# Kernel tuning notes

Hardware: AMD Instinct MI355X
Metric: run time of the kernel (lower is better)

The kernel has to match this reference:

```python
import jax, jax.numpy as jnp
import numpy as np
import math

B, N, C = 16, 4096, 256
HEADS, HD, SR, FF = 8, 32, 4, 3


def _ln(x, g, b):
    mu = jnp.mean(x, -1, keepdims=True)
    var = jnp.mean((x - mu) ** 2, -1, keepdims=True)
    return (x - mu) / jnp.sqrt(var + 1e-5) * g + b


def _interp(v, out):
    # torch F.interpolate(mode='linear', align_corners=False) along axis 1 of (B,L,C)
    L = v.shape[1]
    c = jnp.clip((jnp.arange(out, dtype=v.dtype) + 0.5) * (L / out) - 0.5, 0.0, L - 1.0)
    i0 = jnp.floor(c).astype(jnp.int32)
    i1 = jnp.minimum(i0 + 1, L - 1)
    w = (c - i0.astype(v.dtype))[None, :, None]
    return v[:, i0] * (1.0 - w) + v[:, i1] * w


def _conv(x, w, b, stride, pad=0, groups=1):
    y = jax.lax.conv_general_dilated(x, w, (stride, stride), ((pad, pad), (pad, pad)),
                                     feature_group_count=groups,
                                     dimension_numbers=('NCHW', 'OIHW', 'NCHW'))
    return y + b[None, :, None, None]


def _lin_attn(q_bhnd, k, v, pe, scale_sp, Wdwc, bdwc, n_kv):
    # NOTE: raw reshape (B,h,N,d)->(B,N,C) as in the torch source (layout quirk kept)
    q = q_bhnd.reshape(B, N, C)
    k = k + pe
    q = jax.nn.relu(q) + 1e-6
    k = jax.nn.relu(k) + 1e-6
    q = q / scale_sp
    k = k / scale_sp
    qn = jnp.linalg.norm(q, axis=-1, keepdims=True)
    kn = jnp.linalg.norm(k, axis=-1, keepdims=True)
    q = q ** FF
    k = k ** FF
    q = q / jnp.linalg.norm(q, axis=-1, keepdims=True) * qn
    k = k / jnp.linalg.norm(k, axis=-1, keepdims=True) * kn
    q = q.reshape(B, N, HEADS, HD).transpose(0, 2, 1, 3)        # (B,h,N,d)
    k = k.reshape(B, n_kv, HEADS, HD).transpose(0, 2, 1, 3)     # (B,h,n,d)
    v = v.reshape(B, n_kv, HEADS, HD).transpose(0, 2, 1, 3)
    km = jnp.mean(k, axis=2)                                     # (B,h,d)
    z = 1.0 / (jnp.einsum('bhnd,bhd->bhn', q, km) + 1e-6)
    s = N ** -0.5
    kv = jnp.einsum('bhnd,bhne->bhde', k * s, v * s)             # (B,h,d,d)
    x = jnp.einsum('bhnd,bhde->bhne', q, kv) * z[..., None]
    v2 = _interp(v.reshape(B, n_kv, C), N)                       # raw reshape quirk kept
    Hs = int(math.isqrt(N))
    x = x.transpose(0, 2, 1, 3).reshape(B, N, C)
    v2 = v2.reshape(B * HEADS, Hs, Hs, HD).transpose(0, 3, 1, 2)  # raw reshape quirk kept
    dv = _conv(v2, Wdwc, bdwc, 1, pad=2, groups=HD).reshape(B, C, N).transpose(0, 2, 1)
    return x + dv


def reference(x, Wq, bq, Wsr1, bsr1, g1, b1, Wsr2, bsr2, g2, b2,
              Wkv1, bkv1, Wkv2, bkv2, pe1, pe2, Wproj, bproj,
              Wdwc, bdwc, scale, H, W):
    q = (x @ Wq.T + bq).reshape(B, N, HEADS, HD).transpose(0, 2, 1, 3)
    x_ = x.transpose(0, 2, 1).reshape(B, C, H, W)
    x1 = jax.nn.gelu(_ln(_conv(x_, Wsr1, bsr1, SR).reshape(B, C, -1).transpose(0, 2, 1), g1, b1), approximate=False)
    x2 = jax.nn.gelu(_ln(_conv(x_, Wsr2, bsr2, SR // 2).reshape(B, C, -1).transpose(0, 2, 1), g2, b2), approximate=False)
    h1, h2 = H // SR, 2 * H // SR
    # 1x1 kv convs as linears; then replicate torch's raw reshape of the NCHW conv output
    y1 = (x1.reshape(B, h1, h1, C) @ Wkv1.T + bkv1).transpose(0, 3, 1, 2).reshape(B, h1, h1, 2 * C).reshape(B, -1, 2, C)
    y2 = (x2.reshape(B, h2, h2, C) @ Wkv2.T + bkv2).transpose(0, 3, 1, 2).reshape(B, h2, h2, 2 * C).reshape(B, -1, 2, C)
    k1, v1 = y1[:, :, 0], y1[:, :, 1]
    k2, v2 = y2[:, :, 0], y2[:, :, 1]
    scale_sp = jax.nn.softplus(scale)
    a1 = _lin_attn(q, k1, v1, pe1, scale_sp, Wdwc, bdwc, N // SR ** 2)
    a2 = _lin_attn(q, k2, v2, pe2, scale_sp, Wdwc, bdwc, 4 * N // SR ** 2)
    return jnp.concatenate([a1, a2], axis=-1) @ Wproj.T + bproj


def setup_inputs() -> dict:
    key = jax.random.key(0)
    ks = jax.random.split(key, 12)
    r = lambda k, s: jax.random.normal(k, s, dtype=jnp.float32) * 0.02
    z = lambda s: jnp.zeros(s, jnp.float32)
    return dict(
        x=jax.random.normal(ks[0], (B, N, C), dtype=jnp.float32),
        Wq=r(ks[1], (C, C)), bq=z((C,)),
        Wsr1=r(ks[2], (C, C, SR, SR)), bsr1=z((C,)),
        g1=jnp.ones((C,), jnp.float32), b1=z((C,)),
        Wsr2=r(ks[3], (C, C, SR // 2, SR // 2)), bsr2=z((C,)),
        g2=jnp.ones((C,), jnp.float32), b2=z((C,)),
        Wkv1=r(ks[4], (2 * C, C)), bkv1=z((2 * C,)),
        Wkv2=r(ks[5], (2 * C, C)), bkv2=z((2 * C,)),
        pe1=r(ks[6], (1, N // (SR * SR), C)),
        pe2=r(ks[7], (1, 4 * N // (SR * SR), C)),
        Wproj=r(ks[8], (C, 2 * C)), bproj=z((C,)),
        Wdwc=r(ks[9], (HD, 1, 5, 5)), bdwc=z((HD,)),
        scale=r(ks[10], (1, 1, C)),
        H=64, W=64,
    )
```

## Files before the change

### kernel.cpp

```cpp
#include <hip/hip_runtime.h>
#include <hip/hip_bf16.h>
#include <cmath>

constexpr int cB = 16;
constexpr int cN = 4096;
constexpr int cC = 256;

typedef __attribute__((ext_vector_type(8))) short short8;
typedef __attribute__((ext_vector_type(4))) float f32x4;

__device__ inline unsigned short bfr(float f) {
  __hip_bfloat16 h = __float2bfloat16(f);
  return *(unsigned short*)&h;
}
__device__ inline float u16tof(unsigned short u) {
  unsigned int v = ((unsigned int)u) << 16;
  return __builtin_bit_cast(float, v);
}

constexpr size_t oWQB    = 0;
constexpr size_t oW1B    = oWQB    + 32768;
constexpr size_t oW2B    = oW1B    + 524288;
constexpr size_t oWKV1B  = oW2B    + 131072;
constexpr size_t oWKV2B  = oWKV1B  + 65536;
constexpr size_t oWPROJB = oWKV2B  + 65536;
constexpr size_t oINVSP  = oWPROJB + 65536;
constexpr size_t oKM1    = oINVSP  + 1024;
constexpr size_t oKV1M   = oKM1    + 4096;
constexpr size_t oKM2    = oKV1M   + 131072;
constexpr size_t oKV2M   = oKM2    + 4096;
constexpr size_t oKVP    = oKV2M   + 131072;
constexpr size_t oKMP    = oKVP    + 524288;
constexpr size_t oQBUF   = oKMP    + 16384;
constexpr size_t oV1G    = oQBUF   + 16777216;
constexpr size_t oV2G    = oV1G    + 1048576;
constexpr size_t oU      = oV2G    + 4194304;
constexpr size_t oP1     = oU;
constexpr size_t oX1B    = oU + 4194304;
constexpr size_t oY1     = oU + 4718592;
constexpr size_t oK1P    = oU;
constexpr size_t oX2     = oU;
constexpr size_t oY2     = oU  + 4194304;
constexpr size_t oX2B    = oU  + 12582912;
constexpr size_t oK2P    = oU;
constexpr size_t oAB     = oU;

__global__ void cast_bf16_k(const float* __restrict__ src, __hip_bfloat16* __restrict__ dst, int n) {
  int idx = blockIdx.x*256 + threadIdx.x;
  if (idx < n) dst[idx] = __float2bfloat16(src[idx]);
}

__global__ void pack_conv_bf16(const float* __restrict__ src, __hip_bfloat16* __restrict__ dst, int KHW) {
  int idx = blockIdx.x*256 + threadIdx.x;
  if (idx >= 65536*KHW) return;
  int ci = idx & 255;
  int rest = idx >> 8;
  int p = rest % KHW, co = rest / KHW;
  dst[idx] = __float2bfloat16(src[((size_t)co*256 + ci)*KHW + p]);
}

__global__ void softplus_inv_k(const float* __restrict__ s, float* __restrict__ inv) {
  int c = threadIdx.x;
  float v = s[c];
  float sp = (v > 20.f) ? v : log1pf(expf(v));
  inv[c] = 1.f/sp;
}

template<int TM, int TN, int AMODE, int ADT, int EPI>
__global__ __launch_bounds__(256) void gmfma(
    const void* __restrict__ Asrc, const __hip_bfloat16* __restrict__ Bp,
    const float* __restrict__ bias, float* __restrict__ Cout,
    int M, int N, int K, int ldb)
{
  constexpr int APASS = TM/32, BPASS = TN/32;
  constexpr int WGM = (TM==128) ? 2 : ((TN==64) ? 2 : 1);
  constexpr int WGN = 4/WGM;
  constexpr int WM = TM/WGM, WN = TN/WGN;
  constexpr int FM = WM/16, FN = WN/16;
  __shared__ char smem[(TM+TN)*128];
  char* As = smem;
  char* Bs = smem + TM*128;
  const int tid  = threadIdx.x;
  const int row0 = blockIdx.x * TM;
  const int col0 = blockIdx.y * TN;
  const int kbase = blockIdx.z * K;
  const int kq = tid & 7, rl = tid >> 3;
  const int w = tid >> 6, lane = tid & 63;
  const int wr = (WGM==2) ? (w>>1) : 0;
  const int wc = (WGM==2) ? (w&1)  : w;

  f32x4 acc[FM][FN] = {};
  short8 aS[APASS], bS[BPASS];

  auto loadA = [&](int k0) {
    int ka = kbase + k0;
    #pragma unroll
    for (int p = 0; p < APASS; ++p) {
      int r = row0 + rl + p*32;
      const char* ap;
      if (AMODE == 0) {
        if (ADT == 0) ap = (const char*)((const float*)Asrc + (size_t)r*K + k0 + kq*8);
        else          ap = (const char*)((const __hip_bfloat16*)Asrc + (size_t)r*K + k0 + kq*8);
      } else if (AMODE == 1) {
        int b = r >> 8, mm = r & 255;
        int my = mm >> 4, mx = mm & 15;
        int ch = ka >> 8, ky = ch >> 2, kx = ch & 3;
        int tok = (4*my + ky)*64 + 4*mx + kx;
        ap = (const char*)((const float*)Asrc + ((size_t)(b*4096 + tok))*256 + (ka & 255) + kq*8);
      } else {
        int b = r >> 10, mm = r & 1023;
        int my = mm >> 5, mx = mm & 31;
        int ch = ka >> 8, ky = ch >> 1, kx = ch & 1;
        int tok = (2*my + ky)*64 + 2*mx + kx;
        ap = (const char*)((const float*)Asrc + ((size_t)(b*4096 + tok))*256 + (ka & 255) + kq*8);
      }
      if (ADT == 0) {
        float4 v0 = *(const float4*)ap;
        float4 v1 = *(const float4*)(ap + 16);
        short8 s;
        s[0] = (short)bfr(v0.x); s[1] = (short)bfr(v0.y);
        s[2] = (short)bfr(v0.z); s[3] = (short)bfr(v0.w);
        s[4] = (short)bfr(v1.x); s[5] = (short)bfr(v1.y);
        s[6] = (short)bfr(v1.z); s[7] = (short)bfr(v1.w);
        aS[p] = s;
      } else {
        aS[p] = *(const short8*)ap;
      }
    }
  };
  auto loadB = [&](int k0) {
    #pragma unroll
    for (int p = 0; p < BPASS; ++p) {
      int n = col0 + rl + p*32;
      bS[p] = *(const short8*)(Bp + (size_t)n*ldb + kbase + k0 + kq*8);
    }
  };

  loadA(0); loadB(0);
  for (int k0 = 0; k0 < K; k0 += 64) {
    #pragma unroll
    for (int p = 0; p < APASS; ++p) {
      int r = rl + p*32;
      *(short8*)(As + r*128 + ((kq*16) ^ ((r&7)<<4))) = aS[p];
    }
    #pragma unroll
    for (int p = 0; p < BPASS; ++p) {
      int n = rl + p*32;
      *(short8*)(Bs + n*128 + ((kq*16) ^ ((n&7)<<4))) = bS[p];
    }
    __syncthreads();
    if (k0 + 64 < K) { loadA(k0 + 64); loadB(k0 + 64); }
    #pragma unroll
    for (int ks = 0; ks < 2; ++ks) {
      short8 af[FM], bfv[FN];
      #pragma unroll
      for (int i = 0; i < FM; ++i) {
        int r = wr*WM + i*16 + (lane & 15);
        af[i] = *(const short8*)(As + r*128 + ((ks*64 + (lane>>4)*16) ^ ((r&7)<<4)));
      }
      #pragma unroll
      for (int j = 0; j < FN; ++j) {
        int n = wc*WN + j*16 + (lane & 15);
        bfv[j] = *(const short8*)(Bs + n*128 + ((ks*64 + (lane>>4)*16) ^ ((n&7)<<4)));
      }
      #pragma unroll
      for (int i = 0; i < FM; ++i)
        #pragma unroll
        for (int j = 0; j < FN; ++j)
          acc[i][j] = __builtin_amdgcn_mfma_f32_16x16x32_bf16(af[i], bfv[j], acc[i][j], 0, 0, 0);
    }
    __syncthreads();
  }

  #pragma unroll
  for (int i = 0; i < FM; ++i) {
    #pragma unroll
    for (int j = 0; j < FN; ++j) {
      int cc = col0 + wc*WN + j*16 + (lane & 15);
      float bval = (EPI == 2 || EPI == 3) ? 0.f : bias[cc];
      #pragma unroll
      for (int rg = 0; rg < 4; ++rg) {
        int rr = row0 + wr*WM + i*16 + (lane>>4)*4 + rg;
        float v = acc[i][j][rg] + bval;
        if (EPI == 0) {
          Cout[(size_t)rr*N + cc] = v;
        } else if (EPI == 1) {
          int b = rr >> 12, n = rr & 4095;
          int h = cc >> 5, d = cc & 31;
          Cout[((size_t)(b*4096 + h*512 + (n >> 3)))*256 + (n & 7)*32 + d] = v;
        } else if (EPI == 2) {
          Cout[(size_t)rr*N + cc] += v;
        } else if (EPI == 3) {
          Cout[(size_t)blockIdx.z*((size_t)M*N) + (size_t)rr*N + cc] = v;
        } else {
          int b = rr >> 12, n = rr & 4095;
          int h = cc >> 5, d = cc & 31;
          ((__hip_bfloat16*)Cout)[((size_t)(b*4096 + h*512 + (n >> 3)))*256 + (n & 7)*32 + d] =
              __float2bfloat16(v);
        }
      }
    }
  }
}

__global__ __launch_bounds__(256) void row_powernorm(float* __restrict__ x,
    const float* __restrict__ inv_sp, int rows)
{
  int row = blockIdx.x*4 + (threadIdx.x >> 6);
  if (row >= rows) return;
  int lane = threadIdx.x & 63;
  float* p = x + (size_t)row*256 + lane*4;
  float4 v = *(float4*)p;
  const float4 is = *(const float4*)(inv_sp + lane*4);
  float r0 = (fmaxf(v.x,0.f)+1e-6f)*is.x;
  float r1 = (fmaxf(v.y,0.f)+1e-6f)*is.y;
  float r2 = (fmaxf(v.z,0.f)+1e-6f)*is.z;
  float r3 = (fmaxf(v.w,0.f)+1e-6f)*is.w;
  float s2 = r0*r0+r1*r1+r2*r2+r3*r3;
  #pragma unroll
  for (int o = 1; o < 64; o <<= 1) s2 += __shfl_xor(s2, o, 64);
  float c0 = r0*r0*r0, c1 = r1*r1*r1, c2 = r2*r2*r2, c3 = r3*r3*r3;
  float s6 = c0*c0+c1*c1+c2*c2+c3*c3;
  #pragma unroll
  for (int o = 1; o < 64; o <<= 1) s6 += __shfl_xor(s6, o, 64);
  float f = sqrtf(s2/s6);
  v.x = c0*f; v.y = c1*f; v.z = c2*f; v.w = c3*f;
  *(float4*)p = v;
}

__global__ __launch_bounds__(256) void ln_gelu_sum4(const float* __restrict__ P,
    const float* __restrict__ bias, const float* __restrict__ g, const float* __restrict__ bb,
    __hip_bfloat16* __restrict__ outb, int rows)
{
  const size_t PS = (size_t)rows*256;
  int row = blockIdx.x*4 + (threadIdx.x >> 6);
  if (row >= rows) return;
  int lane = threadIdx.x & 63;
  const float* p = P + (size_t)row*256 + lane*4;
  float4 v0 = *(const float4*)p;
  float4 v1 = *(const float4*)(p + PS);
  float4 v2 = *(const float4*)(p + 2*PS);
  float4 v3 = *(const float4*)(p + 3*PS);
  float4 bsv = *(const float4*)(bias + lane*4);
  float4 v;
  v.x = v0.x+v1.x+v2.x+v3.x+bsv.x;
  v.y = v0.y+v1.y+v2.y+v3.y+bsv.y;
  v.z = v0.z+v1.z+v2.z+v3.z+bsv.z;
  v.w = v0.w+v1.w+v2.w+v3.w+bsv.w;
  float s = v.x+v.y+v.z+v.w;
  #pragma unroll
  for (int o = 1; o < 64; o <<= 1) s += __shfl_xor(s, o, 64);
  float mu = s*(1.f/256.f);
  float d0 = v.x-mu, d1 = v.y-mu, d2 = v.z-mu, d3 = v.w-mu;
  float q = d0*d0+d1*d1+d2*d2+d3*d3;
  #pragma unroll
  for (int o = 1; o < 64; o <<= 1) q += __shfl_xor(q, o, 64);
  float rstd = rsqrtf(q*(1.f/256.f) + 1e-5f);
  float4 gv = *(const float4*)(g + lane*4);
  float4 bv = *(const float4*)(bb + lane*4);
  float y0 = d0*rstd*gv.x + bv.x;
  float y1 = d1*rstd*gv.y + bv.y;
  float y2 = d2*rstd*gv.z + bv.z;
  float y3 = d3*rstd*gv.w + bv.w;
  const float k = 0.70710678118654752f;
  ushort4 u;
  u.x = bfr(0.5f*y0*(1.f+erff(y0*k)));
  u.y = bfr(0.5f*y1*(1.f+erff(y1*k)));
  u.z = bfr(0.5f*y2*(1.f+erff(y2*k)));
  u.w = bfr(0.5f*y3*(1.f+erff(y3*k)));
  *(ushort4*)(outb + (size_t)row*256 + lane*4) = u;
}

__global__ __launch_bounds__(256) void ln_gelu_b(const float* __restrict__ x,
    const float* __restrict__ g, const float* __restrict__ bb,
    __hip_bfloat16* __restrict__ outb, int rows)
{
  int row = blockIdx.x*4 + (threadIdx.x >> 6);
  if (row >= rows) return;
  int lane = threadIdx.x & 63;
  const float* p = x + (size_t)row*256 + lane*4;
  float4 v = *(const float4*)p;
  float s = v.x+v.y+v.z+v.w;
  #pragma unroll
  for (int o = 1; o < 64; o <<= 1) s += __shfl_xor(s, o, 64);
  float mu = s*(1.f/256.f);
  float d0 = v.x-mu, d1 = v.y-mu, d2 = v.z-mu, d3 = v.w-mu;
  float q = d0*d0+d1*d1+d2*d2+d3*d3;
  #pragma unroll
  for (int o = 1; o < 64; o <<= 1) q += __shfl_xor(q, o, 64);
  float rstd = rsqrtf(q*(1.f/256.f) + 1e-5f);
  float4 gv = *(const float4*)(g + lane*4);
  float4 bv = *(const float4*)(bb + lane*4);
  float y0 = d0*rstd*gv.x + bv.x;
  float y1 = d1*rstd*gv.y + bv.y;
  float y2 = d2*rstd*gv.z + bv.z;
  float y3 = d3*rstd*gv.w + bv.w;
  const float k = 0.70710678118654752f;
  ushort4 u;
  u.x = bfr(0.5f*y0*(1.f+erff(y0*k)));
  u.y = bfr(0.5f*y1*(1.f+erff(y1*k)));
  u.z = bfr(0.5f*y2*(1.f+erff(y2*k)));
  u.w = bfr(0.5f*y3*(1.f+erff(y3*k)));
  *(ushort4*)(outb + (size_t)row*256 + lane*4) = u;
}

template<int BR>
__global__ __launch_bounds__(256) void gather_kv2(const float* __restrict__ y,
    const float* __restrict__ pe, float* __restrict__ Ko, float* __restrict__ Vo)
{
  constexpr int NKV = (BR == 1) ? 256 : 1024;
  __shared__ float tk[64][65];
  __shared__ float tv[64][65];
  int bid = blockIdx.x;
  int cb = bid & 3;
  int nb = (bid >> 2) % (NKV/64);
  int b  = (bid >> 2) / (NKV/64);
  int n0 = nb*64, c0 = cb*64;
  int tid = threadIdx.x;
  #pragma unroll
  for (int pass = 0; pass < 16; ++pass) {
    int c_l = (tid >> 6)*16 + pass;
    int c = c0 + c_l;
    if (BR == 1) {
      int n_l = tid & 63;
      size_t base = ((size_t)(b*256 + c))*512 + 2*(n0 + n_l);
      tk[c_l][n_l] = y[base];
      tv[c_l][n_l] = y[base + 1];
    } else {
      int u = tid & 31, pp = (tid >> 5) & 1;
      int n_l = 2*u + pp;
      size_t rk = ((size_t)(b*1024 + pp*512 + c))*512 + (size_t)((n0 >> 1) + u);
      tk[c_l][n_l] = y[rk];
      tv[c_l][n_l] = y[rk + (size_t)256*512];
    }
  }
  __syncthreads();
  #pragma unroll
  for (int pass = 0; pass < 16; ++pass) {
    int n_l = (tid >> 6)*16 + pass;
    int c_l = tid & 63;
    int n = n0 + n_l, c = c0 + c_l;
    size_t o = ((size_t)(b*NKV + n))*256 + c;
    Ko[o] = tk[c_l][n_l] + pe[n*256 + c];
    Vo[o] = tv[c_l][n_l];
  }
}

__global__ __launch_bounds__(256) void kmkv_part(const float* __restrict__ kp,
    const float* __restrict__ vg, float* __restrict__ kmp, float* __restrict__ kvp, int nkv)
{
  int g = blockIdx.x;
  int ch = g & 3, bh = g >> 2;
  int b = bh >> 3, h = bh & 7;
  int nchunk = nkv >> 2;
  int tid = threadIdx.x;
  __shared__ float ks[64][32];
  __shared__ float vs[64][32];
  int d  = tid >> 3;
  int e0 = (tid & 7)*4;
  float acc[4] = {0.f,0.f,0.f,0.f};
  float kmacc = 0.f;
  for (int n0 = ch*nchunk; n0 < (ch+1)*nchunk; n0 += 64) {
    #pragma unroll
    for (int i = 0; i < 2; ++i) {
      int f = tid + i*256;
      int nn = f >> 3, q4 = (f & 7)*4;
      size_t base = ((size_t)(b*nkv + n0 + nn))*256 + h*32 + q4;
      *(float4*)&ks[nn][q4] = *(const float4*)(kp + base);
      *(float4*)&vs[nn][q4] = *(const float4*)(vg + base);
    }
    __syncthreads();
    #pragma unroll 8
    for (int nn = 0; nn < 64; ++nn) {
      float kd = ks[nn][d];
      kmacc += kd;
      #pragma unroll
      for (int j = 0; j < 4; ++j) acc[j] += kd * vs[nn][e0+j];
    }
    __syncthreads();
  }
  const float s2c = 1.0f/4096.0f;
  #pragma unroll
  for (int j = 0; j < 4; ++j)
    kvp[(size_t)ch*131072 + ((size_t)bh*32 + e0 + j)*32 + d] = acc[j]*s2c;
  if ((tid & 7) == 0) kmp[ch*4096 + bh*32 + d] = kmacc;
}

__global__ __launch_bounds__(256) void kmkv_red(const float* __restrict__ kmp,
    const float* __restrict__ kvp, float* __restrict__ km, float* __restrict__ kvm, float inv_nkv)
{
  int idx = blockIdx.x*256 + threadIdx.x;
  kvm[idx] = kvp[idx] + kvp[131072 + idx] + kvp[262144 + idx] + kvp[393216 + idx];
  if (idx < 4096)
    km[idx] = (kmp[idx] + kmp[4096 + idx] + kmp[8192 + idx] + kmp[12288 + idx]) * inv_nkv;
}

__global__ __launch_bounds__(512) void attn_mfma(const __hip_bfloat16* __restrict__ q,
    const float* __restrict__ inv_sp,
    const float* __restrict__ km1, const float* __restrict__ kv1,
    const float* __restrict__ km2, const float* __restrict__ kv2,
    __hip_bfloat16* __restrict__ A)
{
  __shared__ __align__(16) char qs[64*512];
  __shared__ __align__(16) char kvs[32*512];
  __shared__ float zsf[2*64*8];
  const int bid = blockIdx.x;
  const int b = bid >> 6, t0 = (bid & 63)*64;
  const int tid = threadIdx.x;

  {
    const float* src = kv1 + (size_t)b*8192;
    for (int i = tid; i < 8192; i += 512) {
      int h = i >> 10, e = (i >> 5) & 31, d = i & 31;
      *(unsigned short*)(kvs + e*512 + ((h*64 + d*2) ^ ((e&7)<<4))) = bfr(src[i]);
    }
  }

  {
    const int h = tid & 7;
    const int t_l = tid >> 3;
    const float* km1p = km1 + b*256 + h*32;
    const float* km2p = km2 + b*256 + h*32;
    const __hip_bfloat16* qp = q + ((size_t)(b*4096 + t0 + t_l))*256 + h*32;
    float cf[32];
    float s2 = 0.f, s6 = 0.f;
    #pragma unroll
    for (int j = 0; j < 4; ++j) {
      short8 qv = *(const short8*)(qp + j*8);
      float4 is0 = *(const float4*)(inv_sp + h*32 + j*8);
      float4 is1 = *(const float4*)(inv_sp + h*32 + j*8 + 4);
      float isv[8] = {is0.x, is0.y, is0.z, is0.w, is1.x, is1.y, is1.z, is1.w};
      #pragma unroll
      for (int k = 0; k < 8; ++k) {
        float val = u16tof((unsigned short)qv[k]);
        float r = (fmaxf(val, 0.f) + 1e-6f) * isv[k];
        s2 += r*r;
        float c = r*r*r;
        s6 += c*c;
        cf[j*8 + k] = c;
      }
    }
    #pragma unroll
    for (int o = 1; o < 8; o <<= 1) {
      s2 += __shfl_xor(s2, o, 64);
      s6 += __shfl_xor(s6, o, 64);
    }
    float f = sqrtf(s2/s6);
    float d1 = 0.f, d2 = 0.f;
    #pragma unroll
    for (int j = 0; j < 8; ++j) {
      float4 k1 = *(const float4*)(km1p + j*4);
      float4 k2 = *(const float4*)(km2p + j*4);
      float q0 = cf[4*j+0]*f, q1 = cf[4*j+1]*f, q2 = cf[4*j+2]*f, q3 = cf[4*j+3]*f;
      cf[4*j+0] = q0; cf[4*j+1] = q1; cf[4*j+2] = q2; cf[4*j+3] = q3;
      d1 += q0*k1.x + q1*k1.y + q2*k1.z + q3*k1.w;
      d2 += q0*k2.x + q1*k2.y + q2*k2.z + q3*k2.w;
    }
    zsf[0*512 + t_l*8 + h] = 1.0f/(d1 + 1e-6f);
    zsf[1*512 + t_l*8 + h] = 1.0f/(d2 + 1e-6f);
    #pragma unroll
    for (int j = 0; j < 4; ++j) {
      short8 s;
      #pragma unroll
      for (int k = 0; k < 8; ++k) s[k] = (short)bfr(cf[j*8+k]);
      *(short8*)(qs + t_l*512 + ((h*64 + j*16) ^ ((t_l&7)<<4))) = s;
    }
  }
  __syncthreads();

  const int h = tid >> 6, l = tid & 63;
  const int lr = l & 15, lk = l >> 4;
  #pragma unroll
  for (int br = 0; br < 2; ++br) {
    if (br == 1) {
      __syncthreads();
      const float* src = kv2 + (size_t)b*8192;
      for (int i = tid; i < 8192; i += 512) {
        int hh = i >> 10, e = (i >> 5) & 31, d = i & 31;
        *(unsigned short*)(kvs + e*512 + ((hh*64 + d*2) ^ ((e&7)<<4))) = bfr(src[i]);
      }
      __syncthreads();
    }
    #pragma unroll
    for (int tt = 0; tt < 4; ++tt) {
      int tr = tt*16 + lr;
      short8 af = *(const short8*)(qs + tr*512 + ((h*64 + lk*16) ^ ((tr&7)<<4)));
      #pragma unroll
      for (int eb = 0; eb < 2; ++eb) {
        int e = eb*16 + lr;
        short8 bf = *(const short8*)(kvs + e*512 + ((h*64 + lk*16) ^ ((e&7)<<4)));
        f32x4 acc = {0.f, 0.f, 0.f, 0.f};
        acc = __builtin_amdgcn_mfma_f32_16x16x32_bf16(af, bf, acc, 0, 0, 0);
        #pragma unroll
        for (int rg = 0; rg < 4; ++rg) {
          int row = lk*4 + rg;
          float z = zsf[br*512 + (tt*16 + row)*8 + h];
          A[((size_t)(b*4096 + t0 + tt*16 + row))*512 + br*256 + h*32 + e] =
              __float2bfloat16(acc[rg]*z);
        }
      }
    }
  }
}

template<int BR>
__global__ __launch_bounds__(256) void interp_img(const float* __restrict__ vg, float* __restrict__ img) {
  constexpr int L    = (BR == 1) ? 256 : 1024;
  constexpr int RPSH = (BR == 1) ? 5 : 7;
  int row = blockIdx.x*4 + (threadIdx.x >> 6);
  int lane = threadIdx.x & 63;
  int b = row >> 12, t = row & 4095;
  float cpos = ((float)t + 0.5f) * ((float)L / 4096.0f) - 0.5f;
  cpos = fminf(fmaxf(cpos, 0.0f), (float)(L-1));
  int i0 = (int)cpos;
  float w = cpos - (float)i0;
  int i1 = (i0 + 1 < L) ? i0 + 1 : L - 1;
  int cc = lane*4;
  int n0 = ((i0 & ((L/8)-1)) << 3) + (cc >> 5), ch0 = ((i0 >> RPSH) << 5) + (cc & 31);
  int n1 = ((i1 & ((L/8)-1)) << 3) + (cc >> 5), ch1 = ((i1 >> RPSH) << 5) + (cc & 31);
  float4 v0 = *(const float4*)(vg + ((size_t)(b*L + n0))*256 + ch0);
  float4 v1 = *(const float4*)(vg + ((size_t)(b*L + n1))*256 + ch1);
  float4 o;
  o.x = v0.x + (v1.x - v0.x)*w;
  o.y = v0.y + (v1.y - v0.y)*w;
  o.z = v0.z + (v1.z - v0.z)*w;
  o.w = v0.w + (v1.w - v0.w)*w;
  size_t off = ((size_t)((b*8 + (t >> 9))*4096 + ((t >> 3) & 63)*64 + (t & 7)*8 + (cc >> 5)))*32 + (cc & 31);
  *(float4*)(img + off) = o;
}

__global__ __launch_bounds__(256) void dwconv_v3(const float* __restrict__ img,
    const float* __restrict__ Wd, const float* __restrict__ bias,
    __hip_bfloat16* __restrict__ A, int broff)
{
  int wg = blockIdx.x;
  int wid = (wg & 7)*1024 + (wg >> 3);
  int y  = wid & 63;
  int be = wid >> 6;
  int tid = threadIdx.x;
  int d = tid & 31, xg = tid >> 5;
  const float* base = img + (size_t)be*131072 + d;
  float w[25];
  #pragma unroll
  for (int i = 0; i < 25; ++i) w[i] = Wd[d*25 + i];
  float acc[8] = {};
  #pragma unroll
  for (int dy = 0; dy < 5; ++dy) {
    int yy = y + dy - 2;
    if (yy >= 0 && yy <= 63) {
      const float* rb = base + yy*2048;
      float in[12];
      #pragma unroll
      for (int i = 0; i < 12; ++i) {
        int xx = xg*8 - 2 + i;
        in[i] = (xx < 0 || xx > 63) ? 0.f : rb[xx*32];
      }
      #pragma unroll
      for (int dx = 0; dx < 5; ++dx) {
        float ww = w[dy*5 + dx];
        #pragma unroll
        for (int j = 0; j < 8; ++j) acc[j] += ww * in[j + dx];
      }
    }
  }
  int b = be >> 3, e = be & 7;
  float bv = bias[d];
  #pragma unroll
  for (int j = 0; j < 8; ++j) {
    size_t o = ((size_t)(b*4096 + y*64 + xg*8 + j))*512 + broff + e*32 + d;
    float cur = __bfloat162float(A[o]);
    A[o] = __float2bfloat16(cur + acc[j] + bv);
  }
}

extern "C" void kernel_launch(void* const* d_in, const int* in_sizes, int n_in,
                              void* d_out, int out_size, void* d_ws, size_t ws_size,
                              hipStream_t stream)
{
  (void)in_sizes; (void)n_in; (void)out_size; (void)ws_size;
  const float* x     = (const float*)d_in[0];
  const float* Wq    = (const float*)d_in[1];
  const float* bq    = (const float*)d_in[2];
  const float* Wsr1  = (const float*)d_in[3];
  const float* bsr1  = (const float*)d_in[4];
  const float* g1    = (const float*)d_in[5];
  const float* b1    = (const float*)d_in[6];
  const float* Wsr2  = (const float*)d_in[7];
  const float* bsr2  = (const float*)d_in[8];
  const float* g2    = (const float*)d_in[9];
  const float* b2    = (const float*)d_in[10];
  const float* Wkv1  = (const float*)d_in[11];
  const float* bkv1  = (const float*)d_in[12];
  const float* Wkv2  = (const float*)d_in[13];
  const float* bkv2  = (const float*)d_in[14];
  const float* pe1   = (const float*)d_in[15];
  const float* pe2   = (const float*)d_in[16];
  const float* Wproj = (const float*)d_in[17];
  const float* bproj = (const float*)d_in[18];
  const float* Wdwc  = (const float*)d_in[19];
  const float* bdwc  = (const float*)d_in[20];
  const float* scale = (const float*)d_in[21];
  float* out = (float*)d_out;
  float* ws  = (float*)d_ws;
  dim3 blk(256);

  __hip_bfloat16* WQB    = (__hip_bfloat16*)(ws + oWQB);
  __hip_bfloat16* W1B    = (__hip_bfloat16*)(ws + oW1B);
  __hip_bfloat16* W2B    = (__hip_bfloat16*)(ws + oW2B);
  __hip_bfloat16* WKV1B  = (__hip_bfloat16*)(ws + oWKV1B);
  __hip_bfloat16* WKV2B  = (__hip_bfloat16*)(ws + oWKV2B);
  __hip_bfloat16* WPROJB = (__hip_bfloat16*)(ws + oWPROJB);
  __hip_bfloat16* X1B    = (__hip_bfloat16*)(ws + oX1B);
  __hip_bfloat16* X2B    = (__hip_bfloat16*)(ws + oX2B);
  __hip_bfloat16* AB     = (__hip_bfloat16*)(ws + oAB);
  __hip_bfloat16* QB     = (__hip_bfloat16*)(ws + oQBUF);
  float*          IMGF   = (float*)(ws + oQBUF);

  cast_bf16_k<<<256,  blk, 0, stream>>>(Wq,    WQB,    65536);
  cast_bf16_k<<<512,  blk, 0, stream>>>(Wkv1,  WKV1B,  131072);
  cast_bf16_k<<<512,  blk, 0, stream>>>(Wkv2,  WKV2B,  131072);
  cast_bf16_k<<<512,  blk, 0, stream>>>(Wproj, WPROJB, 131072);
  pack_conv_bf16<<<4096, blk, 0, stream>>>(Wsr1, W1B, 16);
  pack_conv_bf16<<<1024, blk, 0, stream>>>(Wsr2, W2B, 4);
  softplus_inv_k<<<1, blk, 0, stream>>>(scale, ws + oINVSP);

  gmfma<128,128,0,0,4><<<dim3(512,2), blk, 0, stream>>>(x, WQB, bq, (float*)QB, 65536, 256, 256, 256);

  gmfma<64,64,1,0,3><<<dim3(64,4,4), blk, 0, stream>>>(x, W1B, bsr1, ws+oP1, 4096, 256, 1024, 4096);
  ln_gelu_sum4<<<1024, blk, 0, stream>>>(ws+oP1, bsr1, g1, b1, X1B, 4096);
  gmfma<64,64,0,1,0><<<dim3(64,8), blk, 0, stream>>>(X1B, WKV1B, bkv1, ws+oY1, 4096, 512, 256, 256);
  gather_kv2<1><<<256, blk, 0, stream>>>(ws+oY1, pe1, ws+oK1P, ws+oV1G);
  row_powernorm<<<1024, blk, 0, stream>>>(ws+oK1P, ws+oINVSP, 4096);
  kmkv_part<<<512, blk, 0, stream>>>(ws+oK1P, ws+oV1G, ws+oKMP, ws+oKVP, 256);
  kmkv_red<<<512, blk, 0, stream>>>(ws+oKMP, ws+oKVP, ws+oKM1, ws+oKV1M, 1.0f/256.0f);

  gmfma<64,64,2,0,0><<<dim3(256,4), blk, 0, stream>>>(x, W2B, bsr2, ws+oX2, 16384, 256, 1024, 1024);
  ln_gelu_b<<<4096, blk, 0, stream>>>(ws+oX2, g2, b2, X2B, 16384);
  gmfma<64,64,0,1,0><<<dim3(256,8), blk, 0, stream>>>(X2B, WKV2B, bkv2, ws+oY2, 16384, 512, 256, 256);
  gather_kv2<2><<<1024, blk, 0, stream>>>(ws+oY2, pe2, ws+oK2P, ws+oV2G);
  row_powernorm<<<4096, blk, 0, stream>>>(ws+oK2P, ws+oINVSP, 16384);
  kmkv_part<<<512, blk, 0, stream>>>(ws+oK2P, ws+oV2G, ws+oKMP, ws+oKVP, 1024);
  kmkv_red<<<512, blk, 0, stream>>>(ws+oKMP, ws+oKVP, ws+oKM2, ws+oKV2M, 1.0f/1024.0f);

  attn_mfma<<<1024, dim3(512), 0, stream>>>(QB, ws+oINVSP,
      ws+oKM1, ws+oKV1M, ws+oKM2, ws+oKV2M, AB);

  interp_img<1><<<16384, blk, 0, stream>>>(ws+oV1G, IMGF);
  dwconv_v3<<<cB*8*64, blk, 0, stream>>>(IMGF, Wdwc, bdwc, AB, 0);
  interp_img<2><<<16384, blk, 0, stream>>>(ws+oV2G, IMGF);
  dwconv_v3<<<cB*8*64, blk, 0, stream>>>(IMGF, Wdwc, bdwc, AB, 256);

  gmfma<128,128,0,1,0><<<dim3(512,2), blk, 0, stream>>>(AB, WPROJB, bproj, out, 65536, 256, 512, 512);
}
```

Baseline: 369.4 us.

## Merge weight packing kernels, fold km/kv reduction into attention, halve attention tile

```diff
diff --git a/kernel.cpp b/kernel.cpp
--- a/kernel.cpp
+++ b/kernel.cpp
@@ -25,13 +25,11 @@
 constexpr size_t oWKV2B  = oWKV1B  + 65536;
 constexpr size_t oWPROJB = oWKV2B  + 65536;
 constexpr size_t oINVSP  = oWPROJB + 65536;
-constexpr size_t oKM1    = oINVSP  + 1024;
-constexpr size_t oKV1M   = oKM1    + 4096;
-constexpr size_t oKM2    = oKV1M   + 131072;
-constexpr size_t oKV2M   = oKM2    + 4096;
-constexpr size_t oKVP    = oKV2M   + 131072;
-constexpr size_t oKMP    = oKVP    + 524288;
-constexpr size_t oQBUF   = oKMP    + 16384;
+constexpr size_t oKMP1   = oINVSP  + 1024;
+constexpr size_t oKVP1   = oKMP1   + 16384;
+constexpr size_t oKMP2   = oKVP1   + 524288;
+constexpr size_t oKVP2   = oKMP2   + 16384;
+constexpr size_t oQBUF   = oKVP2   + 524288;
 constexpr size_t oV1G    = oQBUF   + 16777216;
 constexpr size_t oV2G    = oV1G    + 1048576;
 constexpr size_t oU      = oV2G    + 4194304;
@@ -45,25 +43,39 @@
 constexpr size_t oK2P    = oU;
 constexpr size_t oAB     = oU;
 
-__global__ void cast_bf16_k(const float* __restrict__ src, __hip_bfloat16* __restrict__ dst, int n) {
-  int idx = blockIdx.x*256 + threadIdx.x;
-  if (idx < n) dst[idx] = __float2bfloat16(src[idx]);
-}
-
-__global__ void pack_conv_bf16(const float* __restrict__ src, __hip_bfloat16* __restrict__ dst, int KHW) {
-  int idx = blockIdx.x*256 + threadIdx.x;
-  if (idx >= 65536*KHW) return;
-  int ci = idx & 255;
-  int rest = idx >> 8;
-  int p = rest % KHW, co = rest / KHW;
-  dst[idx] = __float2bfloat16(src[((size_t)co*256 + ci)*KHW + p]);
-}
-
-__global__ void softplus_inv_k(const float* __restrict__ s, float* __restrict__ inv) {
-  int c = threadIdx.x;
-  float v = s[c];
-  float sp = (v > 20.f) ? v : log1pf(expf(v));
-  inv[c] = 1.f/sp;
+__global__ __launch_bounds__(256) void pack_all(
+    const float* __restrict__ Wq,   const float* __restrict__ Wkv1,
+    const float* __restrict__ Wkv2, const float* __restrict__ Wproj,
+    const float* __restrict__ Wsr1, const float* __restrict__ Wsr2,
+    const float* __restrict__ scale,
+    __hip_bfloat16* WQB, __hip_bfloat16* WKV1B, __hip_bfloat16* WKV2B,
+    __hip_bfloat16* WPROJB, __hip_bfloat16* W1B, __hip_bfloat16* W2B,
+    float* inv_sp)
+{
+  int bid = blockIdx.x, tid = threadIdx.x;
+  if (bid < 256) {
+    int i = bid*256 + tid; WQB[i] = __float2bfloat16(Wq[i]);
+  } else if (bid < 768) {
+    int i = (bid-256)*256 + tid; WKV1B[i] = __float2bfloat16(Wkv1[i]);
+  } else if (bid < 1280) {
+    int i = (bid-768)*256 + tid; WKV2B[i] = __float2bfloat16(Wkv2[i]);
+  } else if (bid < 1792) {
+    int i = (bid-1280)*256 + tid; WPROJB[i] = __float2bfloat16(Wproj[i]);
+  } else if (bid < 5888) {
+    int i = (bid-1792)*256 + tid;
+    int ci = i & 255, rest = i >> 8;
+    int p = rest & 15, co = rest >> 4;
+    W1B[i] = __float2bfloat16(Wsr1[((size_t)co*256 + ci)*16 + p]);
+  } else if (bid < 6912) {
+    int i = (bid-5888)*256 + tid;
+    int ci = i & 255, rest = i >> 8;
+    int p = rest & 3, co = rest >> 2;
+    W2B[i] = __float2bfloat16(Wsr2[((size_t)co*256 + ci)*4 + p]);
+  } else {
+    float v = scale[tid];
+    float sp = (v > 20.f) ? v : log1pf(expf(v));
+    inv_sp[tid] = 1.f/sp;
+  }
 }
 
 template<int TM, int TN, int AMODE, int ADT, int EPI>
@@ -386,41 +398,31 @@
   if ((tid & 7) == 0) kmp[ch*4096 + bh*32 + d] = kmacc;
 }
 
-__global__ __launch_bounds__(256) void kmkv_red(const float* __restrict__ kmp,
-    const float* __restrict__ kvp, float* __restrict__ km, float* __restrict__ kvm, float inv_nkv)
-{
-  int idx = blockIdx.x*256 + threadIdx.x;
-  kvm[idx] = kvp[idx] + kvp[131072 + idx] + kvp[262144 + idx] + kvp[393216 + idx];
-  if (idx < 4096)
-    km[idx] = (kmp[idx] + kmp[4096 + idx] + kmp[8192 + idx] + kmp[12288 + idx]) * inv_nkv;
-}
-
 __global__ __launch_bounds__(512) void attn_mfma(const __hip_bfloat16* __restrict__ q,
     const float* __restrict__ inv_sp,
-    const float* __restrict__ km1, const float* __restrict__ kv1,
-    const float* __restrict__ km2, const float* __restrict__ kv2,
+    const float* __restrict__ kmp1, const float* __restrict__ kvp1,
+    const float* __restrict__ kmp2, const float* __restrict__ kvp2,
     __hip_bfloat16* __restrict__ A)
 {
-  __shared__ __align__(16) char qs[64*512];
+  __shared__ __align__(16) char qs[32*512];
   __shared__ __align__(16) char kvs[32*512];
-  __shared__ float zsf[2*64*8];
+  __shared__ float zsf[2*32*8];
   const int bid = blockIdx.x;
-  const int b = bid >> 6, t0 = (bid & 63)*64;
+  const int b = bid >> 7, t0 = (bid & 127)*32;
   const int tid = threadIdx.x;
 
-  {
-    const float* src = kv1 + (size_t)b*8192;
-    for (int i = tid; i < 8192; i += 512) {
-      int h = i >> 10, e = (i >> 5) & 31, d = i & 31;
-      *(unsigned short*)(kvs + e*512 + ((h*64 + d*2) ^ ((e&7)<<4))) = bfr(src[i]);
-    }
-  }
-
-  {
+  for (int i = tid; i < 8192; i += 512) {
+    const float* sp = kvp1 + (size_t)b*8192 + i;
+    float v = sp[0] + sp[131072] + sp[262144] + sp[393216];
+    int h = i >> 10, e = (i >> 5) & 31, d = i & 31;
+    *(unsigned short*)(kvs + e*512 + ((h*64 + d*2) ^ ((e&7)<<4))) = bfr(v);
+  }
+
+  if (tid < 256) {
     const int h = tid & 7;
     const int t_l = tid >> 3;
-    const float* km1p = km1 + b*256 + h*32;
-    const float* km2p = km2 + b*256 + h*32;
+    const float* km1p = kmp1 + b*256 + h*32;
+    const float* km2p = kmp2 + b*256 + h*32;
     const __hip_bfloat16* qp = q + ((size_t)(b*4096 + t0 + t_l))*256 + h*32;
     float cf[32];
     float s2 = 0.f, s6 = 0.f;
@@ -449,15 +451,29 @@
     float d1 = 0.f, d2 = 0.f;
     #pragma unroll
     for (int j = 0; j < 8; ++j) {
-      float4 k1 = *(const float4*)(km1p + j*4);
-      float4 k2 = *(const float4*)(km2p + j*4);
+      float4 k1a = *(const float4*)(km1p + j*4);
+      float4 k1b = *(const float4*)(km1p + 4096 + j*4);
+      float4 k1c = *(const float4*)(km1p + 8192 + j*4);
+      float4 k1d = *(const float4*)(km1p + 12288 + j*4);
+      float4 k2a = *(const float4*)(km2p + j*4);
+      float4 k2b = *(const float4*)(km2p + 4096 + j*4);
+      float4 k2c = *(const float4*)(km2p + 8192 + j*4);
+      float4 k2d = *(const float4*)(km2p + 12288 + j*4);
+      float k1x = (k1a.x+k1b.x+k1c.x+k1d.x)*(1.f/256.f);
+      float k1y = (k1a.y+k1b.y+k1c.y+k1d.y)*(1.f/256.f);
+      float k1z = (k1a.z+k1b.z+k1c.z+k1d.z)*(1.f/256.f);
+      float k1w = (k1a.w+k1b.w+k1c.w+k1d.w)*(1.f/256.f);
+      float k2x = (k2a.x+k2b.x+k2c.x+k2d.x)*(1.f/1024.f);
+      float k2y = (k2a.y+k2b.y+k2c.y+k2d.y)*(1.f/1024.f);
+      float k2z = (k2a.z+k2b.z+k2c.z+k2d.z)*(1.f/1024.f);
+      float k2w = (k2a.w+k2b.w+k2c.w+k2d.w)*(1.f/1024.f);
       float q0 = cf[4*j+0]*f, q1 = cf[4*j+1]*f, q2 = cf[4*j+2]*f, q3 = cf[4*j+3]*f;
       cf[4*j+0] = q0; cf[4*j+1] = q1; cf[4*j+2] = q2; cf[4*j+3] = q3;
-      d1 += q0*k1.x + q1*k1.y + q2*k1.z + q3*k1.w;
-      d2 += q0*k2.x + q1*k2.y + q2*k2.z + q3*k2.w;
-    }
-    zsf[0*512 + t_l*8 + h] = 1.0f/(d1 + 1e-6f);
-    zsf[1*512 + t_l*8 + h] = 1.0f/(d2 + 1e-6f);
+      d1 += q0*k1x + q1*k1y + q2*k1z + q3*k1w;
+      d2 += q0*k2x + q1*k2y + q2*k2z + q3*k2w;
+    }
+    zsf[0*256 + t_l*8 + h] = 1.0f/(d1 + 1e-6f);
+    zsf[1*256 + t_l*8 + h] = 1.0f/(d2 + 1e-6f);
     #pragma unroll
     for (int j = 0; j < 4; ++j) {
       short8 s;
@@ -474,15 +490,16 @@
   for (int br = 0; br < 2; ++br) {
     if (br == 1) {
       __syncthreads();
-      const float* src = kv2 + (size_t)b*8192;
       for (int i = tid; i < 8192; i += 512) {
+        const float* sp = kvp2 + (size_t)b*8192 + i;
+        float v = sp[0] + sp[131072] + sp[262144] + sp[393216];
         int hh = i >> 10, e = (i >> 5) & 31, d = i & 31;
-        *(unsigned short*)(kvs + e*512 + ((hh*64 + d*2) ^ ((e&7)<<4))) = bfr(src[i]);
+        *(unsigned short*)(kvs + e*512 + ((hh*64 + d*2) ^ ((e&7)<<4))) = bfr(v);
       }
       __syncthreads();
     }
     #pragma unroll
-    for (int tt = 0; tt < 4; ++tt) {
+    for (int tt = 0; tt < 2; ++tt) {
       int tr = tt*16 + lr;
       short8 af = *(const short8*)(qs + tr*512 + ((h*64 + lk*16) ^ ((tr&7)<<4)));
       #pragma unroll
@@ -494,7 +511,7 @@
         #pragma unroll
         for (int rg = 0; rg < 4; ++rg) {
           int row = lk*4 + rg;
-          float z = zsf[br*512 + (tt*16 + row)*8 + h];
+          float z = zsf[br*256 + (tt*16 + row)*8 + h];
           A[((size_t)(b*4096 + t0 + tt*16 + row))*512 + br*256 + h*32 + e] =
               __float2bfloat16(acc[rg]*z);
         }
@@ -616,13 +633,8 @@
   __hip_bfloat16* QB     = (__hip_bfloat16*)(ws + oQBUF);
   float*          IMGF   = (float*)(ws + oQBUF);
 
-  cast_bf16_k<<<256,  blk, 0, stream>>>(Wq,    WQB,    65536);
-  cast_bf16_k<<<512,  blk, 0, stream>>>(Wkv1,  WKV1B,  131072);
-  cast_bf16_k<<<512,  blk, 0, stream>>>(Wkv2,  WKV2B,  131072);
-  cast_bf16_k<<<512,  blk, 0, stream>>>(Wproj, WPROJB, 131072);
-  pack_conv_bf16<<<4096, blk, 0, stream>>>(Wsr1, W1B, 16);
-  pack_conv_bf16<<<1024, blk, 0, stream>>>(Wsr2, W2B, 4);
-  softplus_inv_k<<<1, blk, 0, stream>>>(scale, ws + oINVSP);
+  pack_all<<<6913, blk, 0, stream>>>(Wq, Wkv1, Wkv2, Wproj, Wsr1, Wsr2, scale,
+      WQB, WKV1B, WKV2B, WPROJB, W1B, W2B, ws + oINVSP);
 
   gmfma<128,128,0,0,4><<<dim3(512,2), blk, 0, stream>>>(x, WQB, bq, (float*)QB, 65536, 256, 256, 256);
 
@@ -631,19 +643,17 @@
   gmfma<64,64,0,1,0><<<dim3(64,8), blk, 0, stream>>>(X1B, WKV1B, bkv1, ws+oY1, 4096, 512, 256, 256);
   gather_kv2<1><<<256, blk, 0, stream>>>(ws+oY1, pe1, ws+oK1P, ws+oV1G);
   row_powernorm<<<1024, blk, 0, stream>>>(ws+oK1P, ws+oINVSP, 4096);
-  kmkv_part<<<512, blk, 0, stream>>>(ws+oK1P, ws+oV1G, ws+oKMP, ws+oKVP, 256);
-  kmkv_red<<<512, blk, 0, stream>>>(ws+oKMP, ws+oKVP, ws+oKM1, ws+oKV1M, 1.0f/256.0f);
+  kmkv_part<<<512, blk, 0, stream>>>(ws+oK1P, ws+oV1G, ws+oKMP1, ws+oKVP1, 256);
 
   gmfma<64,64,2,0,0><<<dim3(256,4), blk, 0, stream>>>(x, W2B, bsr2, ws+oX2, 16384, 256, 1024, 1024);
   ln_gelu_b<<<4096, blk, 0, stream>>>(ws+oX2, g2, b2, X2B, 16384);
   gmfma<64,64,0,1,0><<<dim3(256,8), blk, 0, stream>>>(X2B, WKV2B, bkv2, ws+oY2, 16384, 512, 256, 256);
   gather_kv2<2><<<1024, blk, 0, stream>>>(ws+oY2, pe2, ws+oK2P, ws+oV2G);
   row_powernorm<<<4096, blk, 0, stream>>>(ws+oK2P, ws+oINVSP, 16384);
-  kmkv_part<<<512, blk, 0, stream>>>(ws+oK2P, ws+oV2G, ws+oKMP, ws+oKVP, 1024);
-  kmkv_red<<<512, blk, 0, stream>>>(ws+oKMP, ws+oKVP, ws+oKM2, ws+oKV2M, 1.0f/1024.0f);
-
-  attn_mfma<<<1024, dim3(512), 0, stream>>>(QB, ws+oINVSP,
-      ws+oKM1, ws+oKV1M, ws+oKM2, ws+oKV2M, AB);
+  kmkv_part<<<512, blk, 0, stream>>>(ws+oK2P, ws+oV2G, ws+oKMP2, ws+oKVP2, 1024);
+
+  attn_mfma<<<2048, dim3(512), 0, stream>>>(QB, ws+oINVSP,
+      ws+oKMP1, ws+oKVP1, ws+oKMP2, ws+oKVP2, AB);
 
   interp_img<1><<<16384, blk, 0, stream>>>(ws+oV1G, IMGF);
   dwconv_v3<<<cB*8*64, blk, 0, stream>>>(IMGF, Wdwc, bdwc, AB, 0);
```

Result: slower. 426.2 us (+15.4%).
